# Kernel tuning notes

Hardware: AMD Instinct MI355X
Metric: run time of the kernel (lower is better)

Reference implementation:

```python
import jax, jax.numpy as jnp
import numpy as np

N, E = 50000, 800000
IN, HID, H, OUT, NLAYERS = 128, 32, 4, 1, 3
F_HID = HID * H  # 128, width between layers


def _glorot(key, shape, scale=0.05):
    return jax.random.normal(key, shape, dtype=jnp.float32) * scale


def setup_inputs() -> dict:
    key = jax.random.key(0)
    ks = jax.random.split(key, 20)
    x = jax.random.normal(ks[0], (N, IN), dtype=jnp.float32)
    edge_index = jax.random.randint(ks[1], (2, E), 0, N, dtype=jnp.int64)
    # layer 0 params (in=IN)
    W_l0 = _glorot(ks[2], (IN, F_HID)); b_l0 = jnp.zeros((F_HID,), jnp.float32)
    W_r0 = _glorot(ks[3], (IN, F_HID)); b_r0 = jnp.zeros((F_HID,), jnp.float32)
    att0 = _glorot(ks[4], (H, HID));    bo0 = jnp.zeros((F_HID,), jnp.float32)
    # layers 1..NLAYERS-1 stacked (in=F_HID)
    L = NLAYERS - 1
    W_l = _glorot(ks[5], (L, F_HID, F_HID)); b_l = jnp.zeros((L, F_HID), jnp.float32)
    W_r = _glorot(ks[6], (L, F_HID, F_HID)); b_r = jnp.zeros((L, F_HID), jnp.float32)
    att = _glorot(ks[7], (L, H, HID));        bo = jnp.zeros((L, F_HID), jnp.float32)
    # final linear
    W_f = _glorot(ks[8], (F_HID, OUT)); b_f = jnp.zeros((OUT,), jnp.float32)
    return dict(x=x, edge_index=edge_index,
                W_l0=W_l0, b_l0=b_l0, W_r0=W_r0, b_r0=b_r0, att0=att0, bo0=bo0,
                W_l=W_l, b_l=b_l, W_r=W_r, b_r=b_r, att=att, bo=bo,
                W_f=W_f, b_f=b_f)


def gatv2_layer(x, src, dst, Wl, bl, Wr, br, a, bo):
    # x: [N, Fin] -> [N, H*HID]. PyG GATv2Conv, concat=True, slope=0.2.
    xl = (x @ Wl + bl).reshape(N, H, HID)  # source transform (messages)
    xr = (x @ Wr + br).reshape(N, H, HID)  # target transform
    z = jax.nn.leaky_relu(xl[src] + xr[dst], 0.2)        # [E', H, HID]
    logits = jnp.einsum('ehc,hc->eh', z, a)              # [E', H]
    m = jax.ops.segment_max(logits, dst, num_segments=N)
    m = jnp.where(jnp.isfinite(m), m, 0.0)
    ex = jnp.exp(logits - m[dst])
    denom = jax.ops.segment_sum(ex, dst, num_segments=N)
    alpha = ex / jnp.maximum(denom[dst], 1e-16)          # segment softmax per dst
    out = jax.ops.segment_sum(xl[src] * alpha[:, :, None], dst, num_segments=N)
    return out.reshape(N, F_HID) + bo


def reference(x, edge_index, W_l0, b_l0, W_r0, b_r0, att0, bo0,
              W_l, b_l, W_r, b_r, att, bo, W_f, b_f):
    loop = jnp.arange(N, dtype=edge_index.dtype)  # PyG default add_self_loops=True
    src = jnp.concatenate([edge_index[0], loop])
    dst = jnp.concatenate([edge_index[1], loop])
    # dropout is identity in eval mode
    h = jax.nn.elu(gatv2_layer(x, src, dst, W_l0, b_l0, W_r0, b_r0, att0, bo0))
    for i in range(NLAYERS - 1):
        h = jax.nn.elu(gatv2_layer(h, src, dst, W_l[i], b_l[i], W_r[i], b_r[i], att[i], bo[i]))
    return h @ W_f + b_f  # [N, OUT]
```

## Files before the change

### kernel.cpp

```cpp
#include <hip/hip_runtime.h>
#include <math.h>

#define N_NODES 50000
#define F 128
#define NEDGE 800000
#define NB_SCAN 49

static __device__ __forceinline__ int imin(int a, int b) { return a < b ? a : b; }

__global__ __launch_bounds__(256) void gemm128(
    const float* __restrict__ A,
    const float* __restrict__ Wl, const float* __restrict__ bl,
    const float* __restrict__ Wr, const float* __restrict__ br,
    float* __restrict__ xl, float* __restrict__ xr)
{
    const float* W = blockIdx.y ? Wr : Wl;
    const float* b = blockIdx.y ? br : bl;
    float*       O = blockIdx.y ? xr : xl;

    __shared__ float As[32][68];
    __shared__ float Ws[32][128];

    const int tid = threadIdx.x;
    const int tx = tid & 15, ty = tid >> 4;
    const int R0 = blockIdx.x * 64;

    float acc[4][8];
#pragma unroll
    for (int i = 0; i < 4; ++i)
#pragma unroll
        for (int j = 0; j < 8; ++j) acc[i][j] = 0.f;

    for (int kt = 0; kt < 4; ++kt) {
#pragma unroll
        for (int i = 0; i < 2; ++i) {
            int f = tid + i * 256;
            int row = f >> 3, kq = f & 7;
            int gr = R0 + row;
            float4 v = make_float4(0.f, 0.f, 0.f, 0.f);
            if (gr < N_NODES) v = *(const float4*)&A[gr * F + kt * 32 + kq * 4];
            As[kq * 4 + 0][row] = v.x; As[kq * 4 + 1][row] = v.y;
            As[kq * 4 + 2][row] = v.z; As[kq * 4 + 3][row] = v.w;
        }
#pragma unroll
        for (int i = 0; i < 4; ++i) {
            int f = tid + i * 256;
            int k = f >> 5, cq = f & 31;
            *(float4*)&Ws[k][cq * 4] = *(const float4*)&W[(kt * 32 + k) * F + cq * 4];
        }
        __syncthreads();
#pragma unroll
        for (int k = 0; k < 32; ++k) {
            float4 a4 = *(const float4*)&As[k][ty * 4];
            float4 w0 = *(const float4*)&Ws[k][tx * 8];
            float4 w1 = *(const float4*)&Ws[k][tx * 8 + 4];
            float av[4] = {a4.x, a4.y, a4.z, a4.w};
            float wv[8] = {w0.x, w0.y, w0.z, w0.w, w1.x, w1.y, w1.z, w1.w};
#pragma unroll
            for (int i = 0; i < 4; ++i)
#pragma unroll
                for (int j = 0; j < 8; ++j) acc[i][j] += av[i] * wv[j];
        }
        __syncthreads();
    }
#pragma unroll
    for (int i = 0; i < 4; ++i) {
        int gr = R0 + ty * 4 + i;
        if (gr < N_NODES) {
#pragma unroll
            for (int j = 0; j < 8; ++j) acc[i][j] += b[tx * 8 + j];
            *(float4*)&O[gr * F + tx * 8]     = make_float4(acc[i][0], acc[i][1], acc[i][2], acc[i][3]);
            *(float4*)&O[gr * F + tx * 8 + 4] = make_float4(acc[i][4], acc[i][5], acc[i][6], acc[i][7]);
        }
    }
}

__global__ void k_init_deg(int* __restrict__ deg)
{
    int i = blockIdx.x * blockDim.x + threadIdx.x;
    if (i < N_NODES) deg[i] = 1;
}

__global__ void k_hist(const int* __restrict__ dst, int* __restrict__ deg)
{
    for (int i = blockIdx.x * blockDim.x + threadIdx.x; i < NEDGE;
         i += gridDim.x * blockDim.x)
        atomicAdd(&deg[dst[i]], 1);
}

__global__ __launch_bounds__(1024) void k_reduce(const int* __restrict__ deg, int* __restrict__ bsum)
{
    __shared__ int s[1024];
    int i = blockIdx.x * 1024 + threadIdx.x;
    s[threadIdx.x] = (i < N_NODES) ? deg[i] : 0;
    __syncthreads();
    for (int d = 512; d > 0; d >>= 1) {
        if (threadIdx.x < d) s[threadIdx.x] += s[threadIdx.x + d];
        __syncthreads();
    }
    if (threadIdx.x == 0) bsum[blockIdx.x] = s[0];
}

__global__ void k_scan_bsum(const int* __restrict__ bsum, int* __restrict__ boff, int nb)
{
    if (blockIdx.x == 0 && threadIdx.x == 0) {
        int run = 0;
        for (int bb = 0; bb < nb; ++bb) { boff[bb] = run; run += bsum[bb]; }
    }
}

__global__ __launch_bounds__(1024) void k_scan(const int* __restrict__ deg, const int* __restrict__ boff,
                                               int* __restrict__ off, int* __restrict__ cursor)
{
    __shared__ int s[1024];
    int i = blockIdx.x * 1024 + threadIdx.x;
    int v = (i < N_NODES) ? deg[i] : 0;
    s[threadIdx.x] = v;
    __syncthreads();
    for (int d = 1; d < 1024; d <<= 1) {
        int tv = (threadIdx.x >= d) ? s[threadIdx.x - d] : 0;
        __syncthreads();
        s[threadIdx.x] += tv;
        __syncthreads();
    }
    int excl = s[threadIdx.x] - v + boff[blockIdx.x];
    int i2 = i;
    if (i2 < N_NODES) { off[i2] = excl; cursor[i2] = excl; }
    if (i2 == N_NODES - 1) off[N_NODES] = excl + v;
}

__global__ void k_scatter(const int* __restrict__ src, const int* __restrict__ dst,
                          int* __restrict__ cursor, int* __restrict__ adj)
{
    for (int i = blockIdx.x * blockDim.x + threadIdx.x; i < NEDGE;
         i += gridDim.x * blockDim.x) {
        int p = atomicAdd(&cursor[dst[i]], 1);
        adj[p] = src[i];
    }
}

__global__ void k_selfloop(int* __restrict__ cursor, int* __restrict__ adj)
{
    int i = blockIdx.x * blockDim.x + threadIdx.x;
    if (i < N_NODES) { int p = atomicAdd(&cursor[i], 1); adj[p] = i; }
}

__device__ __forceinline__ float edge_term(const float4 xlc, const float4 xrv,
                                           const float4 attv)
{
    float z0 = xlc.x + xrv.x, z1 = xlc.y + xrv.y;
    float z2 = xlc.z + xrv.z, z3 = xlc.w + xrv.w;
    z0 = fmaxf(z0, 0.f) + 0.2f * fminf(z0, 0.f);
    z1 = fmaxf(z1, 0.f) + 0.2f * fminf(z1, 0.f);
    z2 = fmaxf(z2, 0.f) + 0.2f * fminf(z2, 0.f);
    z3 = fmaxf(z3, 0.f) + 0.2f * fminf(z3, 0.f);
    float term = z0 * attv.x + z1 * attv.y + z2 * attv.z + z3 * attv.w;
    term += __shfl_xor(term, 4);
    term += __shfl_xor(term, 2);
    term += __shfl_xor(term, 1);
    return term;
}

__global__ __launch_bounds__(256) void gat_edge(
    const float* __restrict__ xl, const float* __restrict__ xr,
    const float* __restrict__ att, const float* __restrict__ bo,
    const int* __restrict__ off, const int* __restrict__ adj,
    float* __restrict__ out)
{
    const int node = blockIdx.x * 8 + (threadIdx.x >> 5);
    if (node >= N_NODES) return;
    const int t = threadIdx.x & 31;
    const float4* __restrict__ xl4 = (const float4*)xl;
    const float4 attv = ((const float4*)att)[t];
    const float4 xrv  = ((const float4*)xr)[(size_t)node * 32 + t];
    const int e0 = off[node], e1 = off[node + 1];
    const int deg = e1 - e0;
    const int nq = deg >> 2, rem = deg & 3;
    const int elast = e1 - 1;

    float m = -1e30f, ssum = 0.f;
    float4 acc = make_float4(0.f, 0.f, 0.f, 0.f);

    int base = e0;
    float4 buf0 = xl4[(size_t)adj[imin(base + 0, elast)] * 32 + t];
    float4 buf1 = xl4[(size_t)adj[imin(base + 1, elast)] * 32 + t];
    float4 buf2 = xl4[(size_t)adj[imin(base + 2, elast)] * 32 + t];
    float4 buf3 = xl4[(size_t)adj[imin(base + 3, elast)] * 32 + t];

    for (int q = 0; q < nq; ++q) {
        float4 x0 = buf0, x1 = buf1, x2 = buf2, x3 = buf3;
        base += 4;
        buf0 = xl4[(size_t)adj[imin(base + 0, elast)] * 32 + t];
        buf1 = xl4[(size_t)adj[imin(base + 1, elast)] * 32 + t];
        buf2 = xl4[(size_t)adj[imin(base + 2, elast)] * 32 + t];
        buf3 = xl4[(size_t)adj[imin(base + 3, elast)] * 32 + t];

        float t0 = edge_term(x0, xrv, attv);
        float t1 = edge_term(x1, xrv, attv);
        float t2 = edge_term(x2, xrv, attv);
        float t3 = edge_term(x3, xrv, attv);

        float qm = fmaxf(fmaxf(t0, t1), fmaxf(t2, t3));
        float nm = fmaxf(m, qm);
        float corr = __expf(m - nm);
        float p0 = __expf(t0 - nm);
        float p1 = __expf(t1 - nm);
        float p2 = __expf(t2 - nm);
        float p3 = __expf(t3 - nm);
        m = nm;
        ssum  = ssum  * corr + ((p0 + p1) + (p2 + p3));
        acc.x = acc.x * corr + (p0 * x0.x + p1 * x1.x + p2 * x2.x + p3 * x3.x);
        acc.y = acc.y * corr + (p0 * x0.y + p1 * x1.y + p2 * x2.y + p3 * x3.y);
        acc.z = acc.z * corr + (p0 * x0.z + p1 * x1.z + p2 * x2.z + p3 * x3.z);
        acc.w = acc.w * corr + (p0 * x0.w + p1 * x1.w + p2 * x2.w + p3 * x3.w);
    }

    if (rem > 0) {
        float tt = edge_term(buf0, xrv, attv);
        float d = tt - m, ev = __expf(-fabsf(d));
        float corr = (d > 0.f) ? ev : 1.f, p = (d > 0.f) ? 1.f : ev;
        m = fmaxf(m, tt);
        ssum  = ssum  * corr + p;
        acc.x = acc.x * corr + p * buf0.x;  acc.y = acc.y * corr + p * buf0.y;
        acc.z = acc.z * corr + p * buf0.z;  acc.w = acc.w * corr + p * buf0.w;
    }
    if (rem > 1) {
        float tt = edge_term(buf1, xrv, attv);
        float d = tt - m, ev = __expf(-fabsf(d));
        float corr = (d > 0.f) ? ev : 1.f, p = (d > 0.f) ? 1.f : ev;
        m = fmaxf(m, tt);
        ssum  = ssum  * corr + p;
        acc.x = acc.x * corr + p * buf1.x;  acc.y = acc.y * corr + p * buf1.y;
        acc.z = acc.z * corr + p * buf1.z;  acc.w = acc.w * corr + p * buf1.w;
    }
    if (rem > 2) {
        float tt = edge_term(buf2, xrv, attv);
        float d = tt - m, ev = __expf(-fabsf(d));
        float corr = (d > 0.f) ? ev : 1.f, p = (d > 0.f) ? 1.f : ev;
        m = fmaxf(m, tt);
        ssum  = ssum  * corr + p;
        acc.x = acc.x * corr + p * buf2.x;  acc.y = acc.y * corr + p * buf2.y;
        acc.z = acc.z * corr + p * buf2.z;  acc.w = acc.w * corr + p * buf2.w;
    }

    const float inv = 1.f / ssum;
    const float4 bov = ((const float4*)bo)[t];
    float4 o;
    o.x = acc.x * inv + bov.x;
    o.y = acc.y * inv + bov.y;
    o.z = acc.z * inv + bov.z;
    o.w = acc.w * inv + bov.w;
    o.x = (o.x > 0.f) ? o.x : expm1f(o.x);
    o.y = (o.y > 0.f) ? o.y : expm1f(o.y);
    o.z = (o.z > 0.f) ? o.z : expm1f(o.z);
    o.w = (o.w > 0.f) ? o.w : expm1f(o.w);
    ((float4*)out)[(size_t)node * 32 + t] = o;
}

__global__ void k_final(const float* __restrict__ h, const float* __restrict__ wf,
                        const float* __restrict__ bf, float* __restrict__ out)
{
    int gw = (blockIdx.x * blockDim.x + threadIdx.x) >> 6;
    int lane = threadIdx.x & 63;
    if (gw >= N_NODES) return;
    float v = h[gw * F + lane] * wf[lane] + h[gw * F + 64 + lane] * wf[64 + lane];
    v += __shfl_xor(v, 32); v += __shfl_xor(v, 16); v += __shfl_xor(v, 8);
    v += __shfl_xor(v, 4);  v += __shfl_xor(v, 2);  v += __shfl_xor(v, 1);
    if (lane == 0) out[gw] = v + bf[0];
}

extern "C" void kernel_launch(void* const* d_in, const int* in_sizes, int n_in,
                              void* d_out, int out_size, void* d_ws, size_t ws_size,
                              hipStream_t stream)
{
    const float* x    = (const float*)d_in[0];
    const int*   ei   = (const int*)  d_in[1];
    const float* W_l0 = (const float*)d_in[2];
    const float* b_l0 = (const float*)d_in[3];
    const float* W_r0 = (const float*)d_in[4];
    const float* b_r0 = (const float*)d_in[5];
    const float* att0 = (const float*)d_in[6];
    const float* bo0  = (const float*)d_in[7];
    const float* W_l  = (const float*)d_in[8];
    const float* b_l  = (const float*)d_in[9];
    const float* W_r  = (const float*)d_in[10];
    const float* b_r  = (const float*)d_in[11];
    const float* att  = (const float*)d_in[12];
    const float* bo   = (const float*)d_in[13];
    const float* W_f  = (const float*)d_in[14];
    const float* b_f  = (const float*)d_in[15];
    float* out = (float*)d_out;

    char* ws = (char*)d_ws;
    size_t o = 0;
    auto alloc = [&](size_t bytes) { void* p = ws + o; o += (bytes + 255) & ~(size_t)255; return p; };
    float* xl  = (float*)alloc((size_t)N_NODES * F * 4);
    float* xr  = (float*)alloc((size_t)N_NODES * F * 4);
    float* hb  = (float*)alloc((size_t)N_NODES * F * 4);
    int* deg   = (int*)alloc((size_t)N_NODES * 4);
    int* off   = (int*)alloc((size_t)(N_NODES + 1) * 4);
    int* cur   = (int*)alloc((size_t)N_NODES * 4);
    int* adj   = (int*)alloc((size_t)(NEDGE + N_NODES) * 4);
    int* bsum  = (int*)alloc(64 * 4);
    int* boff  = (int*)alloc(64 * 4);

    const int* srcv = ei;
    const int* dstv = ei + NEDGE;

    k_init_deg<<<(N_NODES + 255) / 256, 256, 0, stream>>>(deg);
    k_hist<<<1024, 256, 0, stream>>>(dstv, deg);
    k_reduce<<<NB_SCAN, 1024, 0, stream>>>(deg, bsum);
    k_scan_bsum<<<1, 64, 0, stream>>>(bsum, boff, NB_SCAN);
    k_scan<<<NB_SCAN, 1024, 0, stream>>>(deg, boff, off, cur);
    k_scatter<<<1024, 256, 0, stream>>>(srcv, dstv, cur, adj);
    k_selfloop<<<(N_NODES + 255) / 256, 256, 0, stream>>>(cur, adj);

    const float* Ain = x;
    for (int l = 0; l < 3; ++l) {
        const float *Wlp, *blp, *Wrp, *brp, *attp, *bop;
        if (l == 0) {
            Wlp = W_l0; blp = b_l0; Wrp = W_r0; brp = b_r0; attp = att0; bop = bo0;
        } else {
            Wlp = W_l + (size_t)(l - 1) * F * F;
            blp = b_l + (size_t)(l - 1) * F;
            Wrp = W_r + (size_t)(l - 1) * F * F;
            brp = b_r + (size_t)(l - 1) * F;
            attp = att + (size_t)(l - 1) * F;
            bop = bo + (size_t)(l - 1) * F;
        }
        gemm128<<<dim3((N_NODES + 63) / 64, 2), 256, 0, stream>>>(
            Ain, Wlp, blp, Wrp, brp, xl, xr);
        gat_edge<<<(N_NODES + 7) / 8, 256, 0, stream>>>(xl, xr, attp, bop, off, adj, hb);
        Ain = hb;
    }

    k_final<<<(N_NODES + 3) / 4, 256, 0, stream>>>(hb, W_f, b_f, out);
}
```

Before: 547.8 us.

## Enlarge GEMM tile, fuse final linear into last GAT layer, memset degree init

The node GEMM now computes 128-row tiles with an 8x8 register block per thread, cutting shared-memory loads per FMA and the number of blocks. The final 128->1 projection is folded into the last edge-aggregation kernel via a template flag, so the last layer's hidden output is never written or reread. The degree-init kernel is replaced by a memset, with the self-loop +1 added inside the scan. The larger GEMM tile raises register pressure and can lower occupancy.

```diff
diff --git a/kernel.cpp b/kernel.cpp
--- a/kernel.cpp
+++ b/kernel.cpp
@@ -18,27 +18,27 @@
     const float* b = blockIdx.y ? br : bl;
     float*       O = blockIdx.y ? xr : xl;
 
-    __shared__ float As[32][68];
-    __shared__ float Ws[32][128];
+    __shared__ float As[32][132];
+    __shared__ float Ws[32][132];
 
     const int tid = threadIdx.x;
     const int tx = tid & 15, ty = tid >> 4;
-    const int R0 = blockIdx.x * 64;
-
-    float acc[4][8];
-#pragma unroll
-    for (int i = 0; i < 4; ++i)
+    const int R0 = blockIdx.x * 128;
+
+    float acc[8][8];
+#pragma unroll
+    for (int i = 0; i < 8; ++i)
 #pragma unroll
         for (int j = 0; j < 8; ++j) acc[i][j] = 0.f;
 
     for (int kt = 0; kt < 4; ++kt) {
 #pragma unroll
-        for (int i = 0; i < 2; ++i) {
+        for (int i = 0; i < 4; ++i) {
             int f = tid + i * 256;
             int row = f >> 3, kq = f & 7;
             int gr = R0 + row;
             float4 v = make_float4(0.f, 0.f, 0.f, 0.f);
-            if (gr < N_NODES) v = *(const float4*)&A[gr * F + kt * 32 + kq * 4];
+            if (gr < N_NODES) v = *(const float4*)&A[(size_t)gr * F + kt * 32 + kq * 4];
             As[kq * 4 + 0][row] = v.x; As[kq * 4 + 1][row] = v.y;
             As[kq * 4 + 2][row] = v.z; As[kq * 4 + 3][row] = v.w;
         }
@@ -46,39 +46,33 @@
         for (int i = 0; i < 4; ++i) {
             int f = tid + i * 256;
             int k = f >> 5, cq = f & 31;
-            *(float4*)&Ws[k][cq * 4] = *(const float4*)&W[(kt * 32 + k) * F + cq * 4];
+            *(float4*)&Ws[k][cq * 4] = *(const float4*)&W[(size_t)(kt * 32 + k) * F + cq * 4];
         }
         __syncthreads();
 #pragma unroll
         for (int k = 0; k < 32; ++k) {
-            float4 a4 = *(const float4*)&As[k][ty * 4];
-            float4 w0 = *(const float4*)&Ws[k][tx * 8];
-            float4 w1 = *(const float4*)&Ws[k][tx * 8 + 4];
-            float av[4] = {a4.x, a4.y, a4.z, a4.w};
-            float wv[8] = {w0.x, w0.y, w0.z, w0.w, w1.x, w1.y, w1.z, w1.w};
-#pragma unroll
-            for (int i = 0; i < 4; ++i)
-#pragma unroll
-                for (int j = 0; j < 8; ++j) acc[i][j] += av[i] * wv[j];
-        }
-        __syncthreads();
-    }
-#pragma unroll
-    for (int i = 0; i < 4; ++i) {
-        int gr = R0 + ty * 4 + i;
+            float a[8], w[8];
+            *(float4*)&a[0] = *(const float4*)&As[k][ty * 8];
+            *(float4*)&a[4] = *(const float4*)&As[k][ty * 8 + 4];
+            *(float4*)&w[0] = *(const float4*)&Ws[k][tx * 8];
+            *(float4*)&w[4] = *(const float4*)&Ws[k][tx * 8 + 4];
+#pragma unroll
+            for (int i = 0; i < 8; ++i)
+#pragma unroll
+                for (int j = 0; j < 8; ++j) acc[i][j] += a[i] * w[j];
+        }
+        __syncthreads();
+    }
+#pragma unroll
+    for (int i = 0; i < 8; ++i) {
+        int gr = R0 + ty * 8 + i;
         if (gr < N_NODES) {
 #pragma unroll
             for (int j = 0; j < 8; ++j) acc[i][j] += b[tx * 8 + j];
-            *(float4*)&O[gr * F + tx * 8]     = make_float4(acc[i][0], acc[i][1], acc[i][2], acc[i][3]);
-            *(float4*)&O[gr * F + tx * 8 + 4] = make_float4(acc[i][4], acc[i][5], acc[i][6], acc[i][7]);
-        }
-    }
-}
-
-__global__ void k_init_deg(int* __restrict__ deg)
-{
-    int i = blockIdx.x * blockDim.x + threadIdx.x;
-    if (i < N_NODES) deg[i] = 1;
+            *(float4*)&O[(size_t)gr * F + tx * 8]     = make_float4(acc[i][0], acc[i][1], acc[i][2], acc[i][3]);
+            *(float4*)&O[(size_t)gr * F + tx * 8 + 4] = make_float4(acc[i][4], acc[i][5], acc[i][6], acc[i][7]);
+        }
+    }
 }
 
 __global__ void k_hist(const int* __restrict__ dst, int* __restrict__ deg)
@@ -92,7 +86,7 @@
 {
     __shared__ int s[1024];
     int i = blockIdx.x * 1024 + threadIdx.x;
-    s[threadIdx.x] = (i < N_NODES) ? deg[i] : 0;
+    s[threadIdx.x] = (i < N_NODES) ? deg[i] + 1 : 0;
     __syncthreads();
     for (int d = 512; d > 0; d >>= 1) {
         if (threadIdx.x < d) s[threadIdx.x] += s[threadIdx.x + d];
@@ -114,7 +108,7 @@
 {
     __shared__ int s[1024];
     int i = blockIdx.x * 1024 + threadIdx.x;
-    int v = (i < N_NODES) ? deg[i] : 0;
+    int v = (i < N_NODES) ? deg[i] + 1 : 0;
     s[threadIdx.x] = v;
     __syncthreads();
     for (int d = 1; d < 1024; d <<= 1) {
@@ -124,9 +118,8 @@
         __syncthreads();
     }
     int excl = s[threadIdx.x] - v + boff[blockIdx.x];
-    int i2 = i;
-    if (i2 < N_NODES) { off[i2] = excl; cursor[i2] = excl; }
-    if (i2 == N_NODES - 1) off[N_NODES] = excl + v;
+    if (i < N_NODES) { off[i] = excl; cursor[i] = excl; }
+    if (i == N_NODES - 1) off[N_NODES] = excl + v;
 }
 
 __global__ void k_scatter(const int* __restrict__ src, const int* __restrict__ dst,
@@ -161,11 +154,13 @@
     return term;
 }
 
+template <int FUSE_FINAL>
 __global__ __launch_bounds__(256) void gat_edge(
     const float* __restrict__ xl, const float* __restrict__ xr,
     const float* __restrict__ att, const float* __restrict__ bo,
     const int* __restrict__ off, const int* __restrict__ adj,
-    float* __restrict__ out)
+    float* __restrict__ out,
+    const float* __restrict__ wf, const float* __restrict__ bf)
 {
     const int node = blockIdx.x * 8 + (threadIdx.x >> 5);
     if (node >= N_NODES) return;
@@ -254,19 +249,16 @@
     o.y = (o.y > 0.f) ? o.y : expm1f(o.y);
     o.z = (o.z > 0.f) ? o.z : expm1f(o.z);
     o.w = (o.w > 0.f) ? o.w : expm1f(o.w);
-    ((float4*)out)[(size_t)node * 32 + t] = o;
-}
-
-__global__ void k_final(const float* __restrict__ h, const float* __restrict__ wf,
-                        const float* __restrict__ bf, float* __restrict__ out)
-{
-    int gw = (blockIdx.x * blockDim.x + threadIdx.x) >> 6;
-    int lane = threadIdx.x & 63;
-    if (gw >= N_NODES) return;
-    float v = h[gw * F + lane] * wf[lane] + h[gw * F + 64 + lane] * wf[64 + lane];
-    v += __shfl_xor(v, 32); v += __shfl_xor(v, 16); v += __shfl_xor(v, 8);
-    v += __shfl_xor(v, 4);  v += __shfl_xor(v, 2);  v += __shfl_xor(v, 1);
-    if (lane == 0) out[gw] = v + bf[0];
+
+    if (FUSE_FINAL) {
+        const float4 wfv = ((const float4*)wf)[t];
+        float v = o.x * wfv.x + o.y * wfv.y + o.z * wfv.z + o.w * wfv.w;
+        v += __shfl_xor(v, 16); v += __shfl_xor(v, 8); v += __shfl_xor(v, 4);
+        v += __shfl_xor(v, 2);  v += __shfl_xor(v, 1);
+        if (t == 0) out[node] = v + bf[0];
+    } else {
+        ((float4*)out)[(size_t)node * 32 + t] = o;
+    }
 }
 
 extern "C" void kernel_launch(void* const* d_in, const int* in_sizes, int n_in,
@@ -307,7 +299,7 @@
     const int* srcv = ei;
     const int* dstv = ei + NEDGE;
 
-    k_init_deg<<<(N_NODES + 255) / 256, 256, 0, stream>>>(deg);
+    hipMemsetAsync(deg, 0, (size_t)N_NODES * 4, stream);
     k_hist<<<1024, 256, 0, stream>>>(dstv, deg);
     k_reduce<<<NB_SCAN, 1024, 0, stream>>>(deg, bsum);
     k_scan_bsum<<<1, 64, 0, stream>>>(bsum, boff, NB_SCAN);
@@ -328,11 +320,15 @@
             attp = att + (size_t)(l - 1) * F;
             bop = bo + (size_t)(l - 1) * F;
         }
-        gemm128<<<dim3((N_NODES + 63) / 64, 2), 256, 0, stream>>>(
+        gemm128<<<dim3((N_NODES + 127) / 128, 2), 256, 0, stream>>>(
             Ain, Wlp, blp, Wrp, brp, xl, xr);
-        gat_edge<<<(N_NODES + 7) / 8, 256, 0, stream>>>(xl, xr, attp, bop, off, adj, hb);
+        if (l < 2) {
+            gat_edge<0><<<(N_NODES + 7) / 8, 256, 0, stream>>>(
+                xl, xr, attp, bop, off, adj, hb, W_f, b_f);
+        } else {
+            gat_edge<1><<<(N_NODES + 7) / 8, 256, 0, stream>>>(
+                xl, xr, attp, bop, off, adj, out, W_f, b_f);
+        }
         Ain = hb;
     }
-
-    k_final<<<(N_NODES + 3) / 4, 256, 0, stream>>>(hb, W_f, b_f, out);
-}
+}
```

Result: no change. 551.1 us (+0.6%).
